# Performance work log

Hardware: AMD Instinct MI355X
Metric: run time of the kernel (lower is better)

The kernel has to match this reference:

```python
import jax, jax.numpy as jnp
import numpy as np

SIGMAS = (15, 40, 80)  # multi-scale Retinex scales; kernel_size = 2*sigma+1


def _gauss1d(ksize, sigma):
    # kornia.filters.get_gaussian_kernel1d: centered, normalized gaussian
    x = jnp.arange(ksize, dtype=jnp.float32) - (ksize - 1) / 2.0
    g = jnp.exp(-(x * x) / (2.0 * sigma * sigma))
    return g / g.sum()


def _gaussian_blur(img, sigma):
    # img: [B,C,H,W]; kornia gaussian_blur2d: separable depthwise conv,
    # reflect padding, kernel_size = 2*sigma+1
    ksize = int(2 * sigma + 1)
    pad = ksize // 2
    C = img.shape[1]
    k = _gauss1d(ksize, float(sigma))
    xp = jnp.pad(img, ((0, 0), (0, 0), (pad, pad), (pad, pad)), mode='reflect')
    kh = jnp.broadcast_to(k.reshape(1, 1, ksize, 1), (C, 1, ksize, 1))
    kw = jnp.broadcast_to(k.reshape(1, 1, 1, ksize), (C, 1, 1, ksize))
    dn = ('NCHW', 'OIHW', 'NCHW')
    y = jax.lax.conv_general_dilated(xp, kh, (1, 1), 'VALID',
                                     dimension_numbers=dn, feature_group_count=C)
    y = jax.lax.conv_general_dilated(y, kw, (1, 1), 'VALID',
                                     dimension_numbers=dn, feature_group_count=C)
    return y


def setup_inputs() -> dict:
    key = jax.random.key(0)
    B, C, H, W = 8, 3, 1024, 1024
    img = jax.random.uniform(key, (B, C, H, W), dtype=jnp.float32)  # positive, log-safe
    sigmas = jnp.broadcast_to(jnp.array(SIGMAS, dtype=jnp.int32), (B, len(SIGMAS)))
    return {"img": img, "sigmas": sigmas}


def reference(img, sigmas):
    # sigmas determine kernel sizes -> must be static (concrete) values.
    # All batch rows share the same sigma set, so the per-batch loop of the
    # original collapses into batched whole-tensor blurs (identical math).
    sig = np.asarray(sigmas)
    S = sig.shape[1]
    x = img.astype(jnp.float32) + 1e-6
    log_x = jnp.log(x)
    acc = jnp.zeros_like(x)
    for j in range(S):  # small fixed loop over scales (S=3)
        ill = _gaussian_blur(x, int(sig[0, j])) + 1e-6
        acc = acc + (log_x - jnp.log(ill))
    retinex = acc / S
    rmin = retinex.min()
    rmax = retinex.max()
    return (retinex - rmin) / (rmax - rmin) * 255.0
```

## Files before the change

### kernel.cpp

```cpp
#include <hip/hip_runtime.h>
#include <math.h>
#include <string.h>

#define W 1024
#define H 1024
#define HW (1024*1024)
#define NP 24

typedef float  f32x4  __attribute__((ext_vector_type(4)));
typedef short  bf16x8 __attribute__((ext_vector_type(8)));

struct Weights { float w[273]; };

#define P1PIT 328
#define P2P80 328
#define P2P40 264
#define P2P15 200



__device__ __forceinline__ unsigned fenc(float f) {
  unsigned u = __float_as_uint(f);
  return (u & 0x80000000u) ? ~u : (u | 0x80000000u);
}
__device__ __forceinline__ float fdec(unsigned e) {
  unsigned u = (e & 0x80000000u) ? (e & 0x7fffffffu) : ~e;
  return __uint_as_float(u);
}
__device__ __forceinline__ unsigned bfbits(float f) {
  unsigned u = __float_as_uint(f);
  return (u + 0x7fffu + ((u >> 16) & 1u)) >> 16;
}

__device__ __forceinline__ void minmax_reduce4(float lmn, float lmx, unsigned* mm, float* red) {
  #pragma unroll
  for (int off = 32; off > 0; off >>= 1) {
    lmn = fminf(lmn, __shfl_xor(lmn, off));
    lmx = fmaxf(lmx, __shfl_xor(lmx, off));
  }
  const int tid = threadIdx.x;
  const int wid = tid >> 6;
  if ((tid & 63) == 0) { red[wid] = lmn; red[4 + wid] = lmx; }
  __syncthreads();
  if (tid == 0) {
    float mn = fminf(fminf(red[0], red[1]), fminf(red[2], red[3]));
    float mx = fmaxf(fmaxf(red[4], red[5]), fmaxf(red[6], red[7]));
    atomicMin(mm, fenc(mn));
    atomicMax(mm + 1, fenc(mx));
  }
}


__global__ void msr_fraginit(Weights wt, ushort* __restrict__ frag, unsigned* __restrict__ mm) {
  const int tid = threadIdx.x;
  if (tid == 0) { mm[0] = 0xFFFFFFFFu; mm[1] = 0u; }
  const int pads[3] = {80, 40, 15};
  const int woff[3] = {0, 161, 242};
  const int t0s[3]  = {11, 13, 15};
  for (int e = tid; e < 3 * 6 * 64; e += 256) {
    const int s = e / 384;
    const int rem = e - s * 384;
    const int k = rem >> 6;
    const int lane = rem & 63;
    const int pad = pads[s];
    const int d = pad + (t0s[s] + 2 * k) * 16 - 256;
    ushort* dst = frag + e * 8;
    for (int j = 0; j < 8; ++j) {
      const int kk = ((lane >> 4) << 3) + j;
      const int c  = lane & 15;
      const int idx = d + kk - c;
      float v = (idx >= 0 && idx <= 2 * pad) ? wt.w[woff[s] + idx] : 0.f;
      dst[j] = (ushort)bfbits(v);
    }
  }
}


template<int NK, int C0, int FB>
__device__ __forceinline__ void h_round(const short* __restrict__ lds,
                                        const bf16x8* __restrict__ fragv,
                                        ushort* __restrict__ pT,
                                        int lane, int rowshort, int x16, int yin) {
  bf16x8 fr[NK];
  #pragma unroll
  for (int k = 0; k < NK; ++k) fr[k] = fragv[(FB + k) * 64 + lane];
  #pragma unroll
  for (int tx = 0; tx < 8; ++tx) {
    f32x4 acc = {0.f, 0.f, 0.f, 0.f};
    #pragma unroll
    for (int k = 0; k < NK; ++k) {
      bf16x8 a = *(const bf16x8*)(lds + rowshort + tx * 16 + C0 + 32 * k);
      acc = __builtin_amdgcn_mfma_f32_16x16x32_bf16(a, fr[k], acc, 0, 0, 0);
    }
    const unsigned lo = bfbits(acc[0]) | (bfbits(acc[1]) << 16);
    const unsigned hi = bfbits(acc[2]) | (bfbits(acc[3]) << 16);
    *(uint2*)(pT + (size_t)(x16 + tx * 16) * 32 + yin) = make_uint2(lo, hi);
  }
}

__global__ __launch_bounds__(128, 3) void msr_hblur3(
    const float* __restrict__ img, ushort* __restrict__ planesT,
    const bf16x8* __restrict__ fragv) {
  __shared__ __align__(16) short lds[32 * P1PIT];
  const int tid = threadIdx.x;
  const int orig = blockIdx.x + (blockIdx.y << 3) + (blockIdx.z << 8);
  const int l = (orig & 7) * 768 + (orig >> 3);
  const int bx = l & 7;
  const int by = (l >> 3) & 31;
  const int bp = l >> 8;
  const int x0 = bx * 128, y0 = by * 32;
  const float* sp = img + (size_t)bp * HW;
  const int row = tid >> 2, c4 = tid & 3;
  const bool interior = (bx >= 1 && bx <= 6);
  #pragma unroll
  for (int it = 0; it < 20; ++it) {
    const int ccpx = 4 * c4 + 16 * it;
    const int gx0 = x0 - 96 + ccpx;
    unsigned lo, hi;
    if (interior || (gx0 >= 0 && gx0 + 4 <= W)) {
      const float4 v = *(const float4*)(sp + (size_t)(y0 + row) * W + gx0);
      lo = bfbits(v.x) | (bfbits(v.y) << 16);
      hi = bfbits(v.z) | (bfbits(v.w) << 16);
    } else {
      unsigned us[4];
      #pragma unroll
      for (int j = 0; j < 4; ++j) {
        int gx = gx0 + j;
        gx = gx < 0 ? -gx : (gx >= W ? 2 * W - 2 - gx : gx);
        us[j] = bfbits(sp[(size_t)(y0 + row) * W + gx]);
      }
      lo = us[0] | (us[1] << 16); hi = us[2] | (us[3] << 16);
    }
    *(uint2*)(lds + row * P1PIT + ccpx) = make_uint2(lo, hi);
  }
  __syncthreads();

  const int lane = tid & 63;
  const int wrow = (tid >> 6) * 16;
  const int q = lane >> 4;
  const int rowshort = (wrow + (lane & 15)) * P1PIT + q * 8;
  const int x16 = x0 + (lane & 15);
  const int yin = wrow + q * 4;
  const size_t sb = (size_t)by * 32768;

  h_round<6, 16, 0>(lds, fragv, planesT + (size_t)(0 * NP + bp) * HW + sb, lane, rowshort, x16, yin);
  h_round<4, 48, 6>(lds, fragv, planesT + (size_t)(1 * NP + bp) * HW + sb, lane, rowshort, x16, yin);
  h_round<2, 80, 12>(lds, fragv, planesT + (size_t)(2 * NP + bp) * HW + sb, lane, rowshort, x16, yin);
}


template<int NCH, int WD>
__device__ __forceinline__ void p2_prefetch(const ushort* __restrict__ pTs, int xrow,
                                            int ystart, int c4, uint4 (&pre)[10]) {
  #pragma unroll
  for (int i = 0; i < NCH; ++i) {
    const int ccpx = 8 * c4 + 32 * i;
    if (ccpx < WD) {
      const int gy = ystart + ccpx;
      if (gy >= 0 && gy + 8 <= H) {
        pre[i] = *(const uint4*)(pTs + (size_t)(gy >> 5) * 32768 + (size_t)xrow * 32 + (gy & 31));
      } else {
        union { ushort u[8]; uint4 v; } t;
        #pragma unroll
        for (int j = 0; j < 8; ++j) {
          int g = gy + j;
          g = g < 0 ? -g : (g >= H ? 2 * H - 2 - g : g);
          t.u[j] = pTs[(size_t)(g >> 5) * 32768 + (size_t)xrow * 32 + (g & 31)];
        }
        pre[i] = t.v;
      }
    }
  }
}

template<int NCH, int WD, int PIT>
__device__ __forceinline__ void p2_wlds(short* __restrict__ lds, int row, int c4,
                                        const uint4 (&pre)[10]) {
  #pragma unroll
  for (int i = 0; i < NCH; ++i) {
    const int ccpx = 8 * c4 + 32 * i;
    if (ccpx < WD) *(uint4*)(lds + row * PIT + ccpx) = pre[i];
  }
}

template<int NK, int PIT, int FB>
__device__ __forceinline__ void p2_convlog(const short* __restrict__ lds,
                                           const bf16x8* __restrict__ fragv,
                                           int lane, int wrow, float* accL) {
  const int rowshort = (wrow + (lane & 15)) * PIT + (lane >> 4) * 8;
  bf16x8 fr[NK];
  #pragma unroll
  for (int k = 0; k < NK; ++k) fr[k] = fragv[(FB + k) * 64 + lane];
  #pragma unroll
  for (int tx = 0; tx < 8; ++tx) {
    f32x4 acc = {0.f, 0.f, 0.f, 0.f};
    #pragma unroll
    for (int k = 0; k < NK; ++k) {
      bf16x8 a = *(const bf16x8*)(lds + rowshort + tx * 16 + 32 * k);
      acc = __builtin_amdgcn_mfma_f32_16x16x32_bf16(a, fr[k], acc, 0, 0, 0);
    }
    #pragma unroll
    for (int r = 0; r < 4; ++r) accL[tx * 4 + r] -= __logf(acc[r] + 2e-6f);
  }
}

__global__ __launch_bounds__(256) __attribute__((amdgpu_waves_per_eu(2, 3)))
void msr_vblur3(
    const ushort* __restrict__ planesT, const float* __restrict__ img,
    float* __restrict__ out, const bf16x8* __restrict__ fragv, unsigned* __restrict__ mm) {
  __shared__ __align__(16) short lds[64 * P2P80];
  __shared__ float red[8];
  const int tid = threadIdx.x;
  const int orig = blockIdx.x + (blockIdx.y << 4) + (blockIdx.z << 7);
  const int l = (orig & 7) * 384 + (orig >> 3);
  const int byt = l & 7;
  const int bxt = (l >> 3) & 15;
  const int bp = l >> 7;
  const int x0 = bxt * 64, y0 = byt * 128;
  const int row = tid >> 2, c4 = tid & 3;
  const int lane = tid & 63;
  const int wrow = (tid >> 6) * 16;
  const int q = lane >> 4;
  const int xb = x0 + wrow + 4 * q;
  const int ycb = y0 + (lane & 15);

  const ushort* pT0 = planesT + (size_t)(0 * NP + bp) * HW;
  const ushort* pT1 = planesT + (size_t)(1 * NP + bp) * HW;
  const ushort* pT2 = planesT + (size_t)(2 * NP + bp) * HW;

  uint4 pre[10];
  p2_prefetch<10, 304>(pT0, x0 + row, y0 - 80, c4, pre);

  float accL[32];
  const float* ip = img + (size_t)bp * HW;
  #pragma unroll
  for (int tx = 0; tx < 8; ++tx) {
    const float4 v = *(const float4*)(ip + (size_t)(ycb + tx * 16) * W + xb);
    accL[tx * 4 + 0] = 3.f * __logf(v.x + 1e-6f);
    accL[tx * 4 + 1] = 3.f * __logf(v.y + 1e-6f);
    accL[tx * 4 + 2] = 3.f * __logf(v.z + 1e-6f);
    accL[tx * 4 + 3] = 3.f * __logf(v.w + 1e-6f);
  }

  p2_wlds<10, 304, P2P80>(lds, row, c4, pre);
  __syncthreads();
  p2_prefetch<8, 240>(pT1, x0 + row, y0 - 48, c4, pre);
  p2_convlog<6, P2P80, 0>(lds, fragv, lane, wrow, accL);
  __syncthreads();
  p2_wlds<8, 240, P2P40>(lds, row, c4, pre);
  __syncthreads();
  p2_prefetch<6, 176>(pT2, x0 + row, y0 - 16, c4, pre);
  p2_convlog<4, P2P40, 6>(lds, fragv, lane, wrow, accL);
  __syncthreads();
  p2_wlds<6, 176, P2P15>(lds, row, c4, pre);
  __syncthreads();
  p2_convlog<2, P2P15, 12>(lds, fragv, lane, wrow, accL);

  float* op = out + (size_t)bp * HW;
  float lmn = 3.4e38f, lmx = -3.4e38f;
  #pragma unroll
  for (int tx = 0; tx < 8; ++tx) {
    #pragma unroll
    for (int r = 0; r < 4; ++r) {
      lmn = fminf(lmn, accL[tx * 4 + r]);
      lmx = fmaxf(lmx, accL[tx * 4 + r]);
    }
    *(float4*)(op + (size_t)(ycb + tx * 16) * W + xb) =
        make_float4(accL[tx * 4 + 0], accL[tx * 4 + 1], accL[tx * 4 + 2], accL[tx * 4 + 3]);
  }
  minmax_reduce4(lmn, lmx, mm, red);
}


__global__ __launch_bounds__(256) void msr_norm(float* __restrict__ out,
                                                const unsigned* __restrict__ mm) {
  const size_t i = ((size_t)blockIdx.x * 256 + threadIdx.x) * 4;
  const float mn = fdec(mm[0]);
  const float mx = fdec(mm[1]);
  const float sc = 255.f / (mx - mn);
  float4 v = *(float4*)(out + i);
  v.x = (v.x - mn) * sc;
  v.y = (v.y - mn) * sc;
  v.z = (v.z - mn) * sc;
  v.w = (v.w - mn) * sc;
  *(float4*)(out + i) = v;
}


static void compute_weights(Weights* wt) {
  memset(wt, 0, sizeof(Weights));
  const int   ntap[3]  = {161, 81, 31};
  const int   off[3]   = {0, 161, 242};
  const float sigma[3] = {80.f, 40.f, 15.f};
  for (int s = 0; s < 3; ++s) {
    const int k = ntap[s];
    float g[161];
    float sum = 0.f;
    for (int i = 0; i < k; ++i) {
      float x = (float)i - (float)(k - 1) * 0.5f;
      g[i] = expf(-(x * x) / (2.f * sigma[s] * sigma[s]));
      sum += g[i];
    }
    const float inv = 1.f / sum;
    for (int i = 0; i < k; ++i) wt->w[off[s] + i] = g[i] * inv;
  }
}


extern "C" void kernel_launch(void* const* d_in, const int* in_sizes, int n_in,
                              void* d_out, int out_size, void* d_ws, size_t ws_size,
                              hipStream_t stream) {
  const float* img = (const float*)d_in[0];
  float* out = (float*)d_out;
  unsigned* mm = (unsigned*)d_ws;
  ushort* frag = (ushort*)((char*)d_ws + 256);
  ushort* planesT = (ushort*)((char*)d_ws + 32768);

  Weights wt;
  compute_weights(&wt);

  msr_fraginit<<<1, 256, 0, stream>>>(wt, frag, mm);
  msr_hblur3<<<dim3(8, 32, NP), 128, 0, stream>>>(img, planesT, (const bf16x8*)frag);
  msr_vblur3<<<dim3(16, 8, NP), 256, 0, stream>>>(planesT, img, out, (const bf16x8*)frag, mm);
  msr_norm<<<(unsigned)((size_t)NP * HW / 1024), 256, 0, stream>>>(out, mm);
}
```

Measured before the change: 267.0 us.

## Load vertical-blur MFMA operands directly from global memory, dropping LDS staging

The vertical blur pass no longer stages the transposed bf16 planes through shared memory with a prefetch/write/sync sequence. Each lane now reads its MFMA A-operand fragments straight from global memory (relying on L1/L2 for reuse across overlapping windows), with a fast path for interior tiles that skips reflect-boundary checks. Removing LDS and barriers lets the occupancy hint rise from 2-3 to 4-5 waves per EU. The trade-off is redundant global loads for overlapping windows and possible register pressure at the higher occupancy target.

New measurement: 407.5 us. 1.53x slower.

```diff
diff --git a/kernel.cpp b/kernel.cpp
--- a/kernel.cpp
+++ b/kernel.cpp
@@ -13,9 +13,6 @@
 struct Weights { float w[273]; };
 
 #define P1PIT 328
-#define P2P80 328
-#define P2P40 264
-#define P2P15 200
 
 
 
@@ -149,54 +146,34 @@
 }
 
 
-template<int NCH, int WD>
-__device__ __forceinline__ void p2_prefetch(const ushort* __restrict__ pTs, int xrow,
-                                            int ystart, int c4, uint4 (&pre)[10]) {
-  #pragma unroll
-  for (int i = 0; i < NCH; ++i) {
-    const int ccpx = 8 * c4 + 32 * i;
-    if (ccpx < WD) {
-      const int gy = ystart + ccpx;
-      if (gy >= 0 && gy + 8 <= H) {
-        pre[i] = *(const uint4*)(pTs + (size_t)(gy >> 5) * 32768 + (size_t)xrow * 32 + (gy & 31));
+template<int NK, int PE, int FB>
+__device__ __forceinline__ void p2g_round(const ushort* __restrict__ pTs,
+                                          const bf16x8* __restrict__ fragv,
+                                          int xa, int ybase, int lane, bool interior,
+                                          float* accL) {
+  bf16x8 fr[NK];
+  #pragma unroll
+  for (int k = 0; k < NK; ++k) fr[k] = fragv[(FB + k) * 64 + lane];
+  const size_t xoff = (size_t)xa << 5;
+  #pragma unroll
+  for (int tx = 0; tx < 8; ++tx) {
+    f32x4 acc = {0.f, 0.f, 0.f, 0.f};
+    #pragma unroll
+    for (int k = 0; k < NK; ++k) {
+      const int y = ybase - PE + tx * 16 + 32 * k;
+      bf16x8 a;
+      if (interior || (unsigned)y <= (unsigned)(H - 8)) {
+        a = *(const bf16x8*)(pTs + (((size_t)(unsigned)(y >> 5)) << 15) + xoff + (y & 31));
       } else {
-        union { ushort u[8]; uint4 v; } t;
+        union { ushort u[8]; bf16x8 v; } t;
         #pragma unroll
         for (int j = 0; j < 8; ++j) {
-          int g = gy + j;
+          int g = y + j;
           g = g < 0 ? -g : (g >= H ? 2 * H - 2 - g : g);
-          t.u[j] = pTs[(size_t)(g >> 5) * 32768 + (size_t)xrow * 32 + (g & 31)];
+          t.u[j] = pTs[(((size_t)(g >> 5)) << 15) + xoff + (g & 31)];
         }
-        pre[i] = t.v;
+        a = t.v;
       }
-    }
-  }
-}
-
-template<int NCH, int WD, int PIT>
-__device__ __forceinline__ void p2_wlds(short* __restrict__ lds, int row, int c4,
-                                        const uint4 (&pre)[10]) {
-  #pragma unroll
-  for (int i = 0; i < NCH; ++i) {
-    const int ccpx = 8 * c4 + 32 * i;
-    if (ccpx < WD) *(uint4*)(lds + row * PIT + ccpx) = pre[i];
-  }
-}
-
-template<int NK, int PIT, int FB>
-__device__ __forceinline__ void p2_convlog(const short* __restrict__ lds,
-                                           const bf16x8* __restrict__ fragv,
-                                           int lane, int wrow, float* accL) {
-  const int rowshort = (wrow + (lane & 15)) * PIT + (lane >> 4) * 8;
-  bf16x8 fr[NK];
-  #pragma unroll
-  for (int k = 0; k < NK; ++k) fr[k] = fragv[(FB + k) * 64 + lane];
-  #pragma unroll
-  for (int tx = 0; tx < 8; ++tx) {
-    f32x4 acc = {0.f, 0.f, 0.f, 0.f};
-    #pragma unroll
-    for (int k = 0; k < NK; ++k) {
-      bf16x8 a = *(const bf16x8*)(lds + rowshort + tx * 16 + 32 * k);
       acc = __builtin_amdgcn_mfma_f32_16x16x32_bf16(a, fr[k], acc, 0, 0, 0);
     }
     #pragma unroll
@@ -204,11 +181,10 @@
   }
 }
 
-__global__ __launch_bounds__(256) __attribute__((amdgpu_waves_per_eu(2, 3)))
+__global__ __launch_bounds__(256) __attribute__((amdgpu_waves_per_eu(4, 5)))
 void msr_vblur3(
     const ushort* __restrict__ planesT, const float* __restrict__ img,
     float* __restrict__ out, const bf16x8* __restrict__ fragv, unsigned* __restrict__ mm) {
-  __shared__ __align__(16) short lds[64 * P2P80];
   __shared__ float red[8];
   const int tid = threadIdx.x;
   const int orig = blockIdx.x + (blockIdx.y << 4) + (blockIdx.z << 7);
@@ -217,19 +193,19 @@
   const int bxt = (l >> 3) & 15;
   const int bp = l >> 7;
   const int x0 = bxt * 64, y0 = byt * 128;
-  const int row = tid >> 2, c4 = tid & 3;
   const int lane = tid & 63;
   const int wrow = (tid >> 6) * 16;
   const int q = lane >> 4;
+  const int c = lane & 15;
+  const int xa = x0 + wrow + c;
+  const int ybase = y0 + q * 8;
   const int xb = x0 + wrow + 4 * q;
-  const int ycb = y0 + (lane & 15);
+  const int ycb = y0 + c;
+  const bool interior = (byt >= 1 && byt <= 6);
 
   const ushort* pT0 = planesT + (size_t)(0 * NP + bp) * HW;
   const ushort* pT1 = planesT + (size_t)(1 * NP + bp) * HW;
   const ushort* pT2 = planesT + (size_t)(2 * NP + bp) * HW;
-
-  uint4 pre[10];
-  p2_prefetch<10, 304>(pT0, x0 + row, y0 - 80, c4, pre);
 
   float accL[32];
   const float* ip = img + (size_t)bp * HW;
@@ -242,19 +218,9 @@
     accL[tx * 4 + 3] = 3.f * __logf(v.w + 1e-6f);
   }
 
-  p2_wlds<10, 304, P2P80>(lds, row, c4, pre);
-  __syncthreads();
-  p2_prefetch<8, 240>(pT1, x0 + row, y0 - 48, c4, pre);
-  p2_convlog<6, P2P80, 0>(lds, fragv, lane, wrow, accL);
-  __syncthreads();
-  p2_wlds<8, 240, P2P40>(lds, row, c4, pre);
-  __syncthreads();
-  p2_prefetch<6, 176>(pT2, x0 + row, y0 - 16, c4, pre);
-  p2_convlog<4, P2P40, 6>(lds, fragv, lane, wrow, accL);
-  __syncthreads();
-  p2_wlds<6, 176, P2P15>(lds, row, c4, pre);
-  __syncthreads();
-  p2_convlog<2, P2P15, 12>(lds, fragv, lane, wrow, accL);
+  p2g_round<6, 80, 0>(pT0, fragv, xa, ybase, lane, interior, accL);
+  p2g_round<4, 48, 6>(pT1, fragv, xa, ybase, lane, interior, accL);
+  p2g_round<2, 16, 12>(pT2, fragv, xa, ybase, lane, interior, accL);
 
   float* op = out + (size_t)bp * HW;
   float lmn = 3.4e38f, lmx = -3.4e38f;
```
